# Kernel tuning notes

Measured on AMD Instinct MI355X. Metric: run time of the kernel, lower is better.

The kernel has to match this reference:

```python
import jax, jax.numpy as jnp
import numpy as np

N_SEQ, N_RES, C_M = 512, 384, 256
C_O, C_Z = 32, 128  # num_outer_channel, num_output_channel
LN_EPS = 1e-5
NORM_EPS = 1e-3


def setup_inputs() -> dict:
    key = jax.random.key(0)
    ks = jax.random.split(key, 8)
    scale = 1.0 / np.sqrt(C_M)
    return {
        "act": jax.random.normal(ks[0], (N_SEQ, N_RES, C_M), dtype=jnp.float32),
        "mask": jax.random.uniform(ks[1], (N_SEQ, N_RES), dtype=jnp.float32),
        "ln_w": jnp.ones((C_M,), dtype=jnp.float32),
        "ln_b": jnp.zeros((C_M,), dtype=jnp.float32),
        "left_w": jax.random.normal(ks[2], (C_O, C_M), dtype=jnp.float32) * scale,
        "left_b": jnp.zeros((C_O,), dtype=jnp.float32),
        "right_w": jax.random.normal(ks[3], (C_O, C_M), dtype=jnp.float32) * scale,
        "right_b": jnp.zeros((C_O,), dtype=jnp.float32),
        "output_w": jax.random.normal(ks[4], (C_O, C_O, C_Z), dtype=jnp.float32) * (1.0 / C_O),
        "output_b": jnp.zeros((C_Z,), dtype=jnp.float32),
    }


def reference(act, mask, ln_w, ln_b, left_w, left_b, right_w, right_b, output_w, output_b):
    # LayerNorm over c_m
    mu = jnp.mean(act, axis=-1, keepdims=True)
    var = jnp.var(act, axis=-1, keepdims=True)
    act_n = (act - mu) * jax.lax.rsqrt(var + LN_EPS) * ln_w + ln_b

    m = mask[..., None]  # [s, r, 1]
    left = m * (jnp.einsum("src,oc->sro", act_n, left_w) + left_b)    # [s, r, co]
    right = m * (jnp.einsum("src,oc->sro", act_n, right_w) + right_b)  # [s, r, co]

    # outer product over sequence dim, then contract with output_w:
    # out[b, d, f] = sum_{a, c, e} left[a, b, c] * right[a, d, e] * w[c, e, f]
    outer = jnp.einsum("abc,ade->bdce", left, right)          # [r, r, co, co]
    out = jnp.einsum("bdce,cef->bdf", outer, output_w) + output_b  # [r, r, c_z]

    norm = jnp.einsum("sb,sd->bd", mask, mask)[..., None]  # [r, r, 1]
    return out / (NORM_EPS + norm)
```

## Files before the change

kernel.cpp:

```cpp
#include <hip/hip_runtime.h>

typedef short short8 __attribute__((ext_vector_type(8)));
typedef float f32x4 __attribute__((ext_vector_type(4)));
typedef unsigned short ushort_t;

#define DEV_INLINE __device__ __forceinline__

constexpr int NSEQ = 512, NRES = 384, CM = 256, CO = 32, CZ = 128;
constexpr float F_LN_EPS = 1e-5f, F_NORM_EPS = 1e-3f;

constexpr size_t WS_LT   = 0;
constexpr size_t WS_RT   = WS_LT + (size_t)12288 * 512 * 2;
constexpr size_t WS_WT   = WS_RT + (size_t)12288 * 512 * 2;
constexpr size_t WS_NORM = WS_WT + (size_t)128 * 1024 * 2;

DEV_INLINE ushort_t f2bf(float x) {
  union { float f; unsigned u; } v; v.f = x;
  unsigned r = v.u + 0x7FFFu + ((v.u >> 16) & 1u);
  return (ushort_t)(r >> 16);
}

DEV_INLINE short8 pack8(float4 a, float4 b) {
  short8 p;
  p[0] = (short)f2bf(a.x); p[1] = (short)f2bf(a.y);
  p[2] = (short)f2bf(a.z); p[3] = (short)f2bf(a.w);
  p[4] = (short)f2bf(b.x); p[5] = (short)f2bf(b.y);
  p[6] = (short)f2bf(b.z); p[7] = (short)f2bf(b.w);
  return p;
}

DEV_INLINE void async16(const void* g, void* l) {
  __builtin_amdgcn_global_load_lds(
      (const __attribute__((address_space(1))) unsigned*)g,
      (__attribute__((address_space(3))) unsigned*)l, 16, 0, 0);
}

__global__ __launch_bounds__(256) void k_wt(const float* __restrict__ W,
                                            ushort_t* __restrict__ WT) {
  int tid = blockIdx.x * 256 + threadIdx.x;
  int f = tid >> 10, ce = tid & 1023;
  WT[tid] = f2bf(W[(size_t)ce * CZ + f]);
}

__global__ __launch_bounds__(256) void k_norm(const float* __restrict__ mask,
                                              float* __restrict__ normM) {
  int b = blockIdx.x * 16 + threadIdx.x;
  int d = blockIdx.y * 16 + threadIdx.y;
  float a0 = 0.f, a1 = 0.f, a2 = 0.f, a3 = 0.f;
  for (int a = 0; a < NSEQ; a += 4) {
    a0 += mask[(size_t)(a + 0) * NRES + b] * mask[(size_t)(a + 0) * NRES + d];
    a1 += mask[(size_t)(a + 1) * NRES + b] * mask[(size_t)(a + 1) * NRES + d];
    a2 += mask[(size_t)(a + 2) * NRES + b] * mask[(size_t)(a + 2) * NRES + d];
    a3 += mask[(size_t)(a + 3) * NRES + b] * mask[(size_t)(a + 3) * NRES + d];
  }
  normM[(size_t)b * NRES + d] = (a0 + a1) + (a2 + a3);
}

__global__ __launch_bounds__(256) void k_lnproj(
    const float* __restrict__ act, const float* __restrict__ mask,
    const float* __restrict__ ln_w, const float* __restrict__ ln_b,
    const float* __restrict__ left_w, const float* __restrict__ left_b,
    const float* __restrict__ right_w, const float* __restrict__ right_b,
    ushort_t* __restrict__ Lt, ushort_t* __restrict__ Rt) {
  __shared__ ushort_t sAct[64 * 256];
  __shared__ ushort_t sW[64 * 256];

  const int t = threadIdx.x;
  const int a0 = blockIdx.x * 64;
  const int b = blockIdx.y;
  const int r = t >> 2, qc = t & 3;

  const float4* arow =
      (const float4*)(act + ((size_t)(a0 + r) * NRES + b) * CM + qc * 64);
  float4 v[16];
  float s = 0.f, ss = 0.f;
#pragma unroll
  for (int j = 0; j < 16; j++) {
    v[j] = arow[j];
    s += v[j].x + v[j].y + v[j].z + v[j].w;
    ss += v[j].x * v[j].x + v[j].y * v[j].y + v[j].z * v[j].z + v[j].w * v[j].w;
  }
  s += __shfl_xor(s, 1);  s += __shfl_xor(s, 2);
  ss += __shfl_xor(ss, 1); ss += __shfl_xor(ss, 2);
  const float mu = s * (1.f / CM);
  const float rs = rsqrtf(ss * (1.f / CM) - mu * mu + F_LN_EPS);

  {
    const int o = r;
    const float4* wrow = (const float4*)((o < 32 ? left_w + (size_t)o * CM
                                                 : right_w + (size_t)(o - 32) * CM) +
                                         qc * 64);
#pragma unroll
    for (int j = 0; j < 8; j++) {
      short8 p = pack8(wrow[2 * j], wrow[2 * j + 1]);
      int chunk = qc * 8 + j;
      *(short8*)&sW[o * 256 + ((chunk ^ (o & 7)) * 8)] = p;
    }
  }

#pragma unroll
  for (int j = 0; j < 8; j++) {
    int cb = qc * 64 + j * 8;
    float4 lw0 = *(const float4*)(ln_w + cb), lw1 = *(const float4*)(ln_w + cb + 4);
    float4 lb0 = *(const float4*)(ln_b + cb), lb1 = *(const float4*)(ln_b + cb + 4);
    float4 x0 = v[2 * j], x1 = v[2 * j + 1], y0, y1;
    y0.x = (x0.x - mu) * rs * lw0.x + lb0.x;
    y0.y = (x0.y - mu) * rs * lw0.y + lb0.y;
    y0.z = (x0.z - mu) * rs * lw0.z + lb0.z;
    y0.w = (x0.w - mu) * rs * lw0.w + lb0.w;
    y1.x = (x1.x - mu) * rs * lw1.x + lb1.x;
    y1.y = (x1.y - mu) * rs * lw1.y + lb1.y;
    y1.z = (x1.z - mu) * rs * lw1.z + lb1.z;
    y1.w = (x1.w - mu) * rs * lw1.w + lb1.w;
    short8 p = pack8(y0, y1);
    int chunk = qc * 8 + j;
    *(short8*)&sAct[r * 256 + ((chunk ^ (r & 7)) * 8)] = p;
  }
  __syncthreads();

  const int lane = t & 63, w = t >> 6;
  const int q = lane >> 4, ln = lane & 15;
  const int mrow = w * 16 + ln;
  f32x4 acc[4] = {{0, 0, 0, 0}, {0, 0, 0, 0}, {0, 0, 0, 0}, {0, 0, 0, 0}};
#pragma unroll
  for (int ks = 0; ks < 8; ks++) {
    int kc = ks * 4 + q;
    short8 af = *(const short8*)&sAct[mrow * 256 + ((kc ^ (mrow & 7)) * 8)];
#pragma unroll
    for (int tn = 0; tn < 4; tn++) {
      int nrow = tn * 16 + ln;
      short8 bf = *(const short8*)&sW[nrow * 256 + ((kc ^ (nrow & 7)) * 8)];
      acc[tn] = __builtin_amdgcn_mfma_f32_16x16x32_bf16(af, bf, acc[tn], 0, 0, 0);
    }
  }

  float mk[4];
#pragma unroll
  for (int reg = 0; reg < 4; reg++) {
    int aL = w * 16 + q * 4 + reg;
    mk[reg] = mask[(size_t)(a0 + aL) * NRES + b];
  }
#pragma unroll
  for (int tn = 0; tn < 4; tn++) {
    int o = tn * 16 + ln;
    float bias = (o < 32) ? left_b[o] : right_b[o - 32];
    ushort_t* dst = (o < 32) ? (Lt + (size_t)(b * 32 + o) * NSEQ + a0)
                             : (Rt + (size_t)(b * 32 + (o - 32)) * NSEQ + a0);
#pragma unroll
    for (int reg = 0; reg < 4; reg++) {
      float val = (acc[tn][reg] + bias) * mk[reg];
      dst[w * 16 + q * 4 + reg] = f2bf(val);
    }
  }
}

__global__ __launch_bounds__(256, 3) void k_opm(
    const ushort_t* __restrict__ Lt, const ushort_t* __restrict__ Rt,
    const ushort_t* __restrict__ WT, const float* __restrict__ normM,
    const float* __restrict__ out_b, float* __restrict__ out) {
  __shared__ ushort_t smem[24576];
  ushort_t* sA = smem;
  ushort_t* sB = smem + 8192;
  ushort_t* sP = smem;
  ushort_t* sW = smem + 16384;

  const int t = threadIdx.x, lane = t & 63, w = t >> 6;
  const int q = lane >> 4, ln = lane & 15;
  const int wm = w & 1, wn = w >> 1;
  const int m0 = blockIdx.x * 128, n0 = blockIdx.y * 128;
  const int srow8 = lane >> 3, schunk = lane & 7;

  f32x4 acc1[4][4];
#pragma unroll
  for (int i = 0; i < 4; i++)
#pragma unroll
    for (int j = 0; j < 4; j++) acc1[i][j] = {0, 0, 0, 0};

  for (int kt = 0; kt < 8; kt++) {
    __syncthreads();
#pragma unroll
    for (int i = 0; i < 4; i++) {
      int rg = w + i * 4;
      int r = rg * 8 + srow8;
      int gc = schunk ^ (r & 7);
      async16(Lt + (size_t)(m0 + r) * NSEQ + kt * 64 + gc * 8, (char*)sA + rg * 1024);
      async16(Rt + (size_t)(n0 + r) * NSEQ + kt * 64 + gc * 8, (char*)sB + rg * 1024);
    }
    __syncthreads();
#pragma unroll
    for (int ks = 0; ks < 2; ks++) {
      int kc = ks * 4 + q;
      short8 af[4], bf[4];
#pragma unroll
      for (int tm = 0; tm < 4; tm++) {
        int rr = wm * 64 + tm * 16 + ln;
        af[tm] = *(const short8*)&sA[rr * 64 + ((kc ^ (rr & 7)) * 8)];
      }
#pragma unroll
      for (int tn = 0; tn < 4; tn++) {
        int rr = wn * 64 + tn * 16 + ln;
        bf[tn] = *(const short8*)&sB[rr * 64 + ((kc ^ (rr & 7)) * 8)];
      }
#pragma unroll
      for (int tm = 0; tm < 4; tm++)
#pragma unroll
        for (int tn = 0; tn < 4; tn++)
          acc1[tm][tn] =
              __builtin_amdgcn_mfma_f32_16x16x32_bf16(af[tm], bf[tn], acc1[tm][tn], 0, 0, 0);
    }
  }

  __syncthreads();
#pragma unroll
  for (int tm = 0; tm < 4; tm++) {
#pragma unroll
    for (int tn = 0; tn < 4; tn++) {
      int pair = (wm * 2 + (tm >> 1)) * 4 + (wn * 2 + (tn >> 1));
      int e = (tn & 1) * 16 + ln;
#pragma unroll
      for (int reg = 0; reg < 4; reg++) {
        int c = (tm & 1) * 16 + q * 4 + reg;
        int ce = c * 32 + e;
        int pos = (ce >> 3) ^ (pair & 7);
        sP[pair * 1024 + pos * 8 + (ce & 7)] = f2bf(acc1[tm][tn][reg]);
      }
    }
  }
  __syncthreads();

  f32x4 acc2[2] = {{0, 0, 0, 0}, {0, 0, 0, 0}};
  for (int kt = 0; kt < 16; kt++) {
    if (kt) __syncthreads();
#pragma unroll
    for (int i = 0; i < 4; i++) {
      int rg = w + i * 4;
      int r = rg * 8 + srow8;
      int gc = schunk ^ (r & 7);
      async16(WT + (size_t)r * 1024 + kt * 64 + gc * 8, (char*)sW + rg * 1024);
    }
    __syncthreads();
#pragma unroll
    for (int ks = 0; ks < 2; ks++) {
      int pchunk = kt * 8 + ks * 4 + q;
      short8 af = *(const short8*)&sP[ln * 1024 + ((pchunk ^ (ln & 7)) * 8)];
      int kc = ks * 4 + q;
#pragma unroll
      for (int tn = 0; tn < 2; tn++) {
        int fr = w * 32 + tn * 16 + ln;
        short8 bf = *(const short8*)&sW[fr * 64 + ((kc ^ (fr & 7)) * 8)];
        acc2[tn] = __builtin_amdgcn_mfma_f32_16x16x32_bf16(af, bf, acc2[tn], 0, 0, 0);
      }
    }
  }

  const int b = blockIdx.x * 4 + q;
#pragma unroll
  for (int reg = 0; reg < 4; reg++) {
    int d = blockIdx.y * 4 + reg;
    float inv = 1.f / (F_NORM_EPS + normM[(size_t)b * NRES + d]);
#pragma unroll
    for (int tn = 0; tn < 2; tn++) {
      int f = w * 32 + tn * 16 + ln;
      out[((size_t)b * NRES + d) * CZ + f] = (acc2[tn][reg] + out_b[f]) * inv;
    }
  }
}

extern "C" void kernel_launch(void* const* d_in, const int* in_sizes, int n_in,
                              void* d_out, int out_size, void* d_ws, size_t ws_size,
                              hipStream_t stream) {
  (void)in_sizes; (void)n_in; (void)out_size; (void)ws_size;
  const float* act      = (const float*)d_in[0];
  const float* mask     = (const float*)d_in[1];
  const float* ln_w     = (const float*)d_in[2];
  const float* ln_b     = (const float*)d_in[3];
  const float* left_w   = (const float*)d_in[4];
  const float* left_b   = (const float*)d_in[5];
  const float* right_w  = (const float*)d_in[6];
  const float* right_b  = (const float*)d_in[7];
  const float* output_w = (const float*)d_in[8];
  const float* output_b = (const float*)d_in[9];
  float* out = (float*)d_out;

  char* ws = (char*)d_ws;
  ushort_t* Lt = (ushort_t*)(ws + WS_LT);
  ushort_t* Rt = (ushort_t*)(ws + WS_RT);
  ushort_t* WT = (ushort_t*)(ws + WS_WT);
  float* normM = (float*)(ws + WS_NORM);

  hipLaunchKernelGGL(k_wt, dim3(512), dim3(256), 0, stream, output_w, WT);
  hipLaunchKernelGGL(k_norm, dim3(24, 24), dim3(16, 16), 0, stream, mask, normM);
  hipLaunchKernelGGL(k_lnproj, dim3(8, 384), dim3(256), 0, stream, act, mask,
                     ln_w, ln_b, left_w, left_b, right_w, right_b, Lt, Rt);
  hipLaunchKernelGGL(k_opm, dim3(96, 96), dim3(256), 0, stream, Lt, Rt, WT,
                     normM, output_b, out);
}
```

Measured before the change: 629.3 us.

## Prepack projection weights to bf16 once and shrink LN-projection tiles to 16 rows

Adds a small kernel that converts left/right projection weights to bf16 once, so each lnproj block no longer re-reads and converts the full 64x256 fp32 weight tile into shared memory. The lnproj block now handles 16 sequence rows instead of 64: each wave keeps its weight fragments in registers and issues one MFMA chain, and results are written as 4-element vector stores. This cuts LDS use and redundant per-block weight conversion and raises the block count. In exchange, every block reloads the packed weights from global or cache and launches one extra small kernel.

```diff
diff --git a/kernel.cpp b/kernel.cpp
--- a/kernel.cpp
+++ b/kernel.cpp
@@ -1,6 +1,7 @@
 #include <hip/hip_runtime.h>
 
 typedef short short8 __attribute__((ext_vector_type(8)));
+typedef short short4v __attribute__((ext_vector_type(4)));
 typedef float f32x4 __attribute__((ext_vector_type(4)));
 typedef unsigned short ushort_t;
 
@@ -13,6 +14,7 @@
 constexpr size_t WS_RT   = WS_LT + (size_t)12288 * 512 * 2;
 constexpr size_t WS_WT   = WS_RT + (size_t)12288 * 512 * 2;
 constexpr size_t WS_NORM = WS_WT + (size_t)128 * 1024 * 2;
+constexpr size_t WS_PW   = WS_NORM + (size_t)384 * 384 * 4;
 
 DEV_INLINE ushort_t f2bf(float x) {
   union { float f; unsigned u; } v; v.f = x;
@@ -40,6 +42,17 @@
   int tid = blockIdx.x * 256 + threadIdx.x;
   int f = tid >> 10, ce = tid & 1023;
   WT[tid] = f2bf(W[(size_t)ce * CZ + f]);
+}
+
+__global__ __launch_bounds__(256) void k_pack(const float* __restrict__ left_w,
+                                              const float* __restrict__ right_w,
+                                              ushort_t* __restrict__ PW) {
+  int id = blockIdx.x * 256 + threadIdx.x;
+  int o = id >> 5, ch = id & 31;
+  const float* src = (o < 32 ? left_w + (size_t)o * CM
+                             : right_w + (size_t)(o - 32) * CM) + ch * 8;
+  float4 a = *(const float4*)src, b = *(const float4*)(src + 4);
+  *(short8*)&PW[(size_t)o * CM + ch * 8] = pack8(a, b);
 }
 
 __global__ __launch_bounds__(256) void k_norm(const float* __restrict__ mask,
@@ -59,48 +72,43 @@
 __global__ __launch_bounds__(256) void k_lnproj(
     const float* __restrict__ act, const float* __restrict__ mask,
     const float* __restrict__ ln_w, const float* __restrict__ ln_b,
-    const float* __restrict__ left_w, const float* __restrict__ left_b,
-    const float* __restrict__ right_w, const float* __restrict__ right_b,
+    const float* __restrict__ left_b, const float* __restrict__ right_b,
+    const ushort_t* __restrict__ PW,
     ushort_t* __restrict__ Lt, ushort_t* __restrict__ Rt) {
-  __shared__ ushort_t sAct[64 * 256];
-  __shared__ ushort_t sW[64 * 256];
+  __shared__ ushort_t sAct[16 * 256];
 
   const int t = threadIdx.x;
-  const int a0 = blockIdx.x * 64;
+  const int a0 = blockIdx.x * 16;
   const int b = blockIdx.y;
-  const int r = t >> 2, qc = t & 3;
+  const int r = t >> 4, c = t & 15;
 
   const float4* arow =
-      (const float4*)(act + ((size_t)(a0 + r) * NRES + b) * CM + qc * 64);
-  float4 v[16];
+      (const float4*)(act + ((size_t)(a0 + r) * NRES + b) * CM + c * 16);
+  float4 v[4];
   float s = 0.f, ss = 0.f;
 #pragma unroll
-  for (int j = 0; j < 16; j++) {
+  for (int j = 0; j < 4; j++) {
     v[j] = arow[j];
     s += v[j].x + v[j].y + v[j].z + v[j].w;
     ss += v[j].x * v[j].x + v[j].y * v[j].y + v[j].z * v[j].z + v[j].w * v[j].w;
   }
   s += __shfl_xor(s, 1);  s += __shfl_xor(s, 2);
+  s += __shfl_xor(s, 4);  s += __shfl_xor(s, 8);
   ss += __shfl_xor(ss, 1); ss += __shfl_xor(ss, 2);
+  ss += __shfl_xor(ss, 4); ss += __shfl_xor(ss, 8);
   const float mu = s * (1.f / CM);
   const float rs = rsqrtf(ss * (1.f / CM) - mu * mu + F_LN_EPS);
 
-  {
-    const int o = r;
-    const float4* wrow = (const float4*)((o < 32 ? left_w + (size_t)o * CM
-                                                 : right_w + (size_t)(o - 32) * CM) +
-                                         qc * 64);
-#pragma unroll
-    for (int j = 0; j < 8; j++) {
-      short8 p = pack8(wrow[2 * j], wrow[2 * j + 1]);
-      int chunk = qc * 8 + j;
-      *(short8*)&sW[o * 256 + ((chunk ^ (o & 7)) * 8)] = p;
-    }
-  }
-
-#pragma unroll
-  for (int j = 0; j < 8; j++) {
-    int cb = qc * 64 + j * 8;
+  const int lane = t & 63, w = t >> 6;
+  const int q = lane >> 4, ln = lane & 15;
+  short8 bfrag[8];
+#pragma unroll
+  for (int ks = 0; ks < 8; ks++)
+    bfrag[ks] = *(const short8*)&PW[(size_t)(w * 16 + ln) * CM + (ks * 4 + q) * 8];
+
+#pragma unroll
+  for (int j = 0; j < 2; j++) {
+    int cb = c * 16 + j * 8;
     float4 lw0 = *(const float4*)(ln_w + cb), lw1 = *(const float4*)(ln_w + cb + 4);
     float4 lb0 = *(const float4*)(ln_b + cb), lb1 = *(const float4*)(ln_b + cb + 4);
     float4 x0 = v[2 * j], x1 = v[2 * j + 1], y0, y1;
@@ -112,46 +120,32 @@
     y1.y = (x1.y - mu) * rs * lw1.y + lb1.y;
     y1.z = (x1.z - mu) * rs * lw1.z + lb1.z;
     y1.w = (x1.w - mu) * rs * lw1.w + lb1.w;
-    short8 p = pack8(y0, y1);
-    int chunk = qc * 8 + j;
-    *(short8*)&sAct[r * 256 + ((chunk ^ (r & 7)) * 8)] = p;
+    int chunk = c * 2 + j;
+    *(short8*)&sAct[r * 256 + ((chunk ^ (r & 7)) * 8)] = pack8(y0, y1);
   }
   __syncthreads();
 
-  const int lane = t & 63, w = t >> 6;
-  const int q = lane >> 4, ln = lane & 15;
-  const int mrow = w * 16 + ln;
-  f32x4 acc[4] = {{0, 0, 0, 0}, {0, 0, 0, 0}, {0, 0, 0, 0}, {0, 0, 0, 0}};
+  f32x4 acc = {0, 0, 0, 0};
 #pragma unroll
   for (int ks = 0; ks < 8; ks++) {
     int kc = ks * 4 + q;
-    short8 af = *(const short8*)&sAct[mrow * 256 + ((kc ^ (mrow & 7)) * 8)];
-#pragma unroll
-    for (int tn = 0; tn < 4; tn++) {
-      int nrow = tn * 16 + ln;
-      short8 bf = *(const short8*)&sW[nrow * 256 + ((kc ^ (nrow & 7)) * 8)];
-      acc[tn] = __builtin_amdgcn_mfma_f32_16x16x32_bf16(af, bf, acc[tn], 0, 0, 0);
-    }
-  }
-
+    short8 af = *(const short8*)&sAct[ln * 256 + ((kc ^ (ln & 7)) * 8)];
+    acc = __builtin_amdgcn_mfma_f32_16x16x32_bf16(af, bfrag[ks], acc, 0, 0, 0);
+  }
+
+  const int o = w * 16 + ln;
   float mk[4];
 #pragma unroll
-  for (int reg = 0; reg < 4; reg++) {
-    int aL = w * 16 + q * 4 + reg;
-    mk[reg] = mask[(size_t)(a0 + aL) * NRES + b];
-  }
-#pragma unroll
-  for (int tn = 0; tn < 4; tn++) {
-    int o = tn * 16 + ln;
-    float bias = (o < 32) ? left_b[o] : right_b[o - 32];
-    ushort_t* dst = (o < 32) ? (Lt + (size_t)(b * 32 + o) * NSEQ + a0)
-                             : (Rt + (size_t)(b * 32 + (o - 32)) * NSEQ + a0);
-#pragma unroll
-    for (int reg = 0; reg < 4; reg++) {
-      float val = (acc[tn][reg] + bias) * mk[reg];
-      dst[w * 16 + q * 4 + reg] = f2bf(val);
-    }
-  }
+  for (int reg = 0; reg < 4; reg++)
+    mk[reg] = mask[(size_t)(a0 + q * 4 + reg) * NRES + b];
+  float bias = (o < 32) ? left_b[o] : right_b[o - 32];
+  ushort_t* dst = (o < 32) ? (Lt + (size_t)(b * 32 + o) * NSEQ)
+                           : (Rt + (size_t)(b * 32 + (o - 32)) * NSEQ);
+  short4v pk;
+#pragma unroll
+  for (int reg = 0; reg < 4; reg++)
+    pk[reg] = (short)f2bf((acc[reg] + bias) * mk[reg]);
+  *(short4v*)&dst[a0 + q * 4] = pk;
 }
 
 __global__ __launch_bounds__(256, 3) void k_opm(
@@ -287,11 +281,13 @@
   ushort_t* Rt = (ushort_t*)(ws + WS_RT);
   ushort_t* WT = (ushort_t*)(ws + WS_WT);
   float* normM = (float*)(ws + WS_NORM);
-
+  ushort_t* PW = (ushort_t*)(ws + WS_PW);
+
+  hipLaunchKernelGGL(k_pack, dim3(8), dim3(256), 0, stream, left_w, right_w, PW);
   hipLaunchKernelGGL(k_wt, dim3(512), dim3(256), 0, stream, output_w, WT);
   hipLaunchKernelGGL(k_norm, dim3(24, 24), dim3(16, 16), 0, stream, mask, normM);
-  hipLaunchKernelGGL(k_lnproj, dim3(8, 384), dim3(256), 0, stream, act, mask,
-                     ln_w, ln_b, left_w, left_b, right_w, right_b, Lt, Rt);
+  hipLaunchKernelGGL(k_lnproj, dim3(32, 384), dim3(256), 0, stream, act, mask,
+                     ln_w, ln_b, left_b, right_b, PW, Lt, Rt);
   hipLaunchKernelGGL(k_opm, dim3(96, 96), dim3(256), 0, stream, Lt, Rt, WT,
                      normM, output_b, out);
 }
```

Measured after the change: 607.8 us. -3.4%, faster.
